# Kernel optimization log

Measured on AMD Instinct MI355X. Metric: run time of the kernel, lower is better.

## Reference

```python
import jax, jax.numpy as jnp
import numpy as np

EMBED_DIM = 1024
NUM_HEADS = 16
HEAD_DIM = EMBED_DIM // NUM_HEADS
B, S = 2, 2048


def setup_inputs() -> dict:
    key = jax.random.key(0)
    ks = jax.random.split(key, 9)
    d = EMBED_DIM
    std = 1.0 / np.sqrt(d)
    inp = {
        "x": jax.random.normal(ks[0], (B, S, d), dtype=jnp.float32),
        "wq": jax.random.normal(ks[1], (d, d), dtype=jnp.float32) * std,
        "bq": jnp.zeros((d,), dtype=jnp.float32),
        "wk": jax.random.normal(ks[2], (d, d), dtype=jnp.float32) * std,
        "bk": jnp.zeros((d,), dtype=jnp.float32),
        "wv": jax.random.normal(ks[3], (d, d), dtype=jnp.float32) * std,
        "bv": jnp.zeros((d,), dtype=jnp.float32),
        "wo": jax.random.normal(ks[4], (d, d), dtype=jnp.float32) * std,
        "bo": jnp.zeros((d,), dtype=jnp.float32),
    }
    return inp


def _split_heads(t):
    # [B,S,D] -> [B,H,S,hd]
    b, s, _ = t.shape
    return t.reshape(b, s, NUM_HEADS, HEAD_DIM).transpose(0, 2, 1, 3)


def reference(x, wq, bq, wk, bk, wv, bv, wo, bo):
    scaling = HEAD_DIM ** -0.5
    q = _split_heads(x @ wq + bq)
    k = _split_heads(x @ wk + bk)
    v = _split_heads(x @ wv + bv)
    # scaled dot-product attention, full [B,H,S,S] scores as in the torch code
    attn = jnp.einsum("bhqd,bhkd->bhqk", q, k) * scaling
    attn = jax.nn.softmax(attn, axis=-1)
    out = jnp.einsum("bhqk,bhkd->bhqd", attn, v)
    out = out.transpose(0, 2, 1, 3).reshape(x.shape[0], x.shape[1], EMBED_DIM)
    out = out @ wo + bo
    return out, attn
```

## Files before the change

### kernel.cpp

```cpp
#include <hip/hip_runtime.h>

#define B_   2
#define S_   2048
#define D_   1024
#define H_   16
#define HD_  64
#define MTOT 4096

typedef __bf16 bf16_t;
typedef bf16_t bf16x8 __attribute__((ext_vector_type(8)));
typedef bf16_t bf16x4 __attribute__((ext_vector_type(4)));
typedef float  f32x4  __attribute__((ext_vector_type(4)));

__device__ __forceinline__ void gl_lds16(const bf16_t* g, bf16_t* l) {
  __builtin_amdgcn_global_load_lds((const __attribute__((address_space(1))) void*)g,
                                   (__attribute__((address_space(3))) void*)l, 16, 0, 0);
}

__global__ void cvt_kernel(const float* __restrict__ in, bf16_t* __restrict__ o) {
  size_t i = ((size_t)blockIdx.x * 256 + threadIdx.x) * 4;
  float4 v = *(const float4*)(in + i);
  bf16x4 p;
  p[0] = (bf16_t)v.x; p[1] = (bf16_t)v.y; p[2] = (bf16_t)v.z; p[3] = (bf16_t)v.w;
  *(bf16x4*)(o + i) = p;
}

__global__ void transpose_kernel(const float* __restrict__ w0, const float* __restrict__ w1,
                                 const float* __restrict__ w2, const float* __restrict__ w3,
                                 bf16_t* __restrict__ t0, bf16_t* __restrict__ t1,
                                 bf16_t* __restrict__ t2, bf16_t* __restrict__ t3) {
  const float* w = blockIdx.z == 0 ? w0 : (blockIdx.z == 1 ? w1 : (blockIdx.z == 2 ? w2 : w3));
  bf16_t*      o = blockIdx.z == 0 ? t0 : (blockIdx.z == 1 ? t1 : (blockIdx.z == 2 ? t2 : t3));
  __shared__ float tile[32][33];
  int bx = blockIdx.x * 32, by = blockIdx.y * 32;
#pragma unroll
  for (int i = threadIdx.y; i < 32; i += 8)
    tile[i][threadIdx.x] = w[(size_t)(by + i) * D_ + bx + threadIdx.x];
  __syncthreads();
#pragma unroll
  for (int i = threadIdx.y; i < 32; i += 8)
    o[(size_t)(bx + i) * D_ + by + threadIdx.x] = (bf16_t)tile[threadIdx.x][i];
}

__device__ __forceinline__ void gemm_core(const bf16_t* __restrict__ A,
                                          const bf16_t* __restrict__ Bt,
                                          bf16_t* sA, bf16_t* sB,
                                          int bm, int bn, f32x4 acc[4][4]) {
  const int t = threadIdx.x;
  const int w = t >> 6, lane = t & 63;
  const int wr = w >> 1, wc = w & 1;
  const int r0 = w * 16 + (lane >> 2);
  const int kk = (lane & 3) * 8;
  const int fr = lane & 15, fg = lane >> 4;

  for (int k0 = 0; k0 < 1024; k0 += 32) {
    __syncthreads();
    gl_lds16(A  + (size_t)(bm + r0)      * 1024 + k0 + kk, sA + w * 512);
    gl_lds16(A  + (size_t)(bm + r0 + 64) * 1024 + k0 + kk, sA + 2048 + w * 512);
    gl_lds16(Bt + (size_t)(bn + r0)      * 1024 + k0 + kk, sB + w * 512);
    gl_lds16(Bt + (size_t)(bn + r0 + 64) * 1024 + k0 + kk, sB + 2048 + w * 512);
    __syncthreads();
    bf16x8 a[4], b[4];
#pragma unroll
    for (int m = 0; m < 4; ++m)
      a[m] = *(const bf16x8*)&sA[(wr * 64 + m * 16 + fr) * 32 + fg * 8];
#pragma unroll
    for (int n = 0; n < 4; ++n)
      b[n] = *(const bf16x8*)&sB[(wc * 64 + n * 16 + fr) * 32 + fg * 8];
#pragma unroll
    for (int m = 0; m < 4; ++m)
#pragma unroll
      for (int n = 0; n < 4; ++n)
        acc[m][n] = __builtin_amdgcn_mfma_f32_16x16x32_bf16(a[m], b[n], acc[m][n], 0, 0, 0);
  }
}

__global__ __launch_bounds__(256) void qkv_gemm(
    const bf16_t* __restrict__ xb,
    const bf16_t* __restrict__ wqT, const bf16_t* __restrict__ wkT, const bf16_t* __restrict__ wvT,
    const float* __restrict__ bq, const float* __restrict__ bk, const float* __restrict__ bv,
    bf16_t* __restrict__ Qb, bf16_t* __restrict__ Kb, bf16_t* __restrict__ Vt) {
  __shared__ bf16_t sA[128 * 32], sB[128 * 32];
  const int bid = blockIdx.x;
  const int nid = (bid & 7) * 96 + (bid >> 3);
  const int z = nid >> 8, rem = nid & 255;
  const int bm = (rem >> 3) * 128, bn = (rem & 7) * 128;
  const bf16_t* Bt   = z == 0 ? wqT : (z == 1 ? wkT : wvT);
  const float*  bias = z == 0 ? bq  : (z == 1 ? bk  : bv);

  f32x4 acc[4][4];
#pragma unroll
  for (int m = 0; m < 4; ++m)
#pragma unroll
    for (int n = 0; n < 4; ++n) acc[m][n] = (f32x4){0.f, 0.f, 0.f, 0.f};

  gemm_core(xb, Bt, sA, sB, bm, bn, acc);

  const int t = threadIdx.x, w = t >> 6, lane = t & 63;
  const int wr = w >> 1, wc = w & 1, fr = lane & 15, fg = lane >> 4;
  if (z <= 1) {
    bf16_t* O = (z == 0) ? Qb : Kb;
#pragma unroll
    for (int m = 0; m < 4; ++m)
#pragma unroll
      for (int n = 0; n < 4; ++n) {
        int col = bn + wc * 64 + n * 16 + fr;
        int h = col >> 6, d = col & 63;
        float bi = bias[col];
#pragma unroll
        for (int j = 0; j < 4; ++j) {
          int row = bm + wr * 64 + m * 16 + fg * 4 + j;
          int bb = row >> 11, s = row & 2047;
          O[(((size_t)(bb * H_ + h)) * S_ + s) * HD_ + d] = (bf16_t)(acc[m][n][j] + bi);
        }
      }
  } else {
#pragma unroll
    for (int m = 0; m < 4; ++m)
#pragma unroll
      for (int n = 0; n < 4; ++n) {
        int col = bn + wc * 64 + n * 16 + fr;
        int h = col >> 6, d = col & 63;
        float bi = bias[col];
        int row0 = bm + wr * 64 + m * 16 + fg * 4;
        int bb = row0 >> 11, s0 = row0 & 2047;
        bf16x4 pk;
#pragma unroll
        for (int j = 0; j < 4; ++j) pk[j] = (bf16_t)(acc[m][n][j] + bi);
        *(bf16x4*)&Vt[(((size_t)(bb * H_ + h)) * HD_ + d) * S_ + s0] = pk;
      }
  }
}

__global__ __launch_bounds__(256) void out_gemm(const bf16_t* __restrict__ Ob,
                                                const bf16_t* __restrict__ woT,
                                                const float* __restrict__ bo,
                                                float* __restrict__ out) {
  __shared__ bf16_t sA[128 * 32], sB[128 * 32];
  const int bid = blockIdx.x;
  const int nid = (bid & 7) * 32 + (bid >> 3);
  const int bm = (nid >> 3) * 128, bn = (nid & 7) * 128;
  f32x4 acc[4][4];
#pragma unroll
  for (int m = 0; m < 4; ++m)
#pragma unroll
    for (int n = 0; n < 4; ++n) acc[m][n] = (f32x4){0.f, 0.f, 0.f, 0.f};

  gemm_core(Ob, woT, sA, sB, bm, bn, acc);

  const int t = threadIdx.x, w = t >> 6, lane = t & 63;
  const int wr = w >> 1, wc = w & 1, fr = lane & 15, fg = lane >> 4;
#pragma unroll
  for (int m = 0; m < 4; ++m)
#pragma unroll
    for (int n = 0; n < 4; ++n) {
      int col = bn + wc * 64 + n * 16 + fr;
      float bi = bo[col];
#pragma unroll
      for (int j = 0; j < 4; ++j) {
        int row = bm + wr * 64 + m * 16 + fg * 4 + j;
        out[(size_t)row * D_ + col] = acc[m][n][j] + bi;
      }
    }
}

__global__ __launch_bounds__(256) void attn_kernel(const bf16_t* __restrict__ Qb,
                                                   const bf16_t* __restrict__ Kb,
                                                   const bf16_t* __restrict__ Vt,
                                                   float* __restrict__ attn,
                                                   bf16_t* __restrict__ Ob) {
  __shared__ bf16_t p_lds[4][16 * 72];
  const int t = threadIdx.x, w = t >> 6, lane = t & 63;
  const int fr = lane & 15, fg = lane >> 4;
  const int bid = blockIdx.x;
  const int nid = (bid & 7) * 128 + (bid >> 3);
  const int qblk = nid & 31, bh = nid >> 5;
  const int bb = bh >> 4, h = bh & 15;
  const int q0 = qblk * 64 + w * 16;

  const bf16_t* Qh = Qb + (size_t)bh * S_ * HD_;
  const bf16_t* Kh = Kb + (size_t)bh * S_ * HD_;
  const bf16_t* Vh = Vt + (size_t)bh * HD_ * S_;

  bf16x8 aq0 = *(const bf16x8*)&Qh[(size_t)(q0 + fr) * HD_ + fg * 8];
  bf16x8 aq1 = *(const bf16x8*)&Qh[(size_t)(q0 + fr) * HD_ + 32 + fg * 8];

  float lsum = 0.f;
  for (int kt = 0; kt < S_; kt += 64) {
#pragma unroll
    for (int c = 0; c < 4; ++c) {
      const bf16_t* kp = &Kh[(size_t)(kt + c * 16 + fr) * HD_ + fg * 8];
      bf16x8 kb0 = *(const bf16x8*)kp;
      bf16x8 kb1 = *(const bf16x8*)(kp + 32);
      f32x4 zz = {0.f, 0.f, 0.f, 0.f};
      __builtin_amdgcn_s_setprio(1);
      zz = __builtin_amdgcn_mfma_f32_16x16x32_bf16(kb0, aq0, zz, 0, 0, 0);
      zz = __builtin_amdgcn_mfma_f32_16x16x32_bf16(kb1, aq1, zz, 0, 0, 0);
      __builtin_amdgcn_s_setprio(0);
#pragma unroll
      for (int j = 0; j < 4; ++j) lsum += __expf(zz[j] * 0.125f);
    }
  }
  lsum += __shfl_xor(lsum, 16, 64);
  lsum += __shfl_xor(lsum, 32, 64);
  const float invq = 1.f / lsum;

  f32x4 oacc[4];
#pragma unroll
  for (int g = 0; g < 4; ++g) oacc[g] = (f32x4){0.f, 0.f, 0.f, 0.f};

  float* attn_base = attn + ((size_t)bh * S_ + q0) * S_;
  for (int kt = 0; kt < S_; kt += 64) {
#pragma unroll
    for (int c = 0; c < 4; ++c) {
      const bf16_t* kp = &Kh[(size_t)(kt + c * 16 + fr) * HD_ + fg * 8];
      bf16x8 kb0 = *(const bf16x8*)kp;
      bf16x8 kb1 = *(const bf16x8*)(kp + 32);
      f32x4 zz = {0.f, 0.f, 0.f, 0.f};
      __builtin_amdgcn_s_setprio(1);
      zz = __builtin_amdgcn_mfma_f32_16x16x32_bf16(kb0, aq0, zz, 0, 0, 0);
      zz = __builtin_amdgcn_mfma_f32_16x16x32_bf16(kb1, aq1, zz, 0, 0, 0);
      __builtin_amdgcn_s_setprio(0);
      f32x4 pv;
      bf16x4 pk;
#pragma unroll
      for (int j = 0; j < 4; ++j) {
        float p = __expf(zz[j] * 0.125f) * invq;
        pv[j] = p; pk[j] = (bf16_t)p;
      }
      *(f32x4*)&attn_base[(size_t)fr * S_ + kt + c * 16 + fg * 4] = pv;
      *(bf16x4*)&p_lds[w][fr * 72 + c * 16 + fg * 4] = pk;
    }
    bf16x8 ap0 = *(const bf16x8*)&p_lds[w][fr * 72 + fg * 8];
    bf16x8 ap1 = *(const bf16x8*)&p_lds[w][fr * 72 + 32 + fg * 8];
#pragma unroll
    for (int g = 0; g < 4; ++g) {
      const bf16_t* vp = &Vh[(size_t)(g * 16 + fr) * S_ + kt + fg * 8];
      bf16x8 b0 = *(const bf16x8*)vp;
      bf16x8 b1 = *(const bf16x8*)(vp + 32);
      __builtin_amdgcn_s_setprio(1);
      oacc[g] = __builtin_amdgcn_mfma_f32_16x16x32_bf16(ap0, b0, oacc[g], 0, 0, 0);
      oacc[g] = __builtin_amdgcn_mfma_f32_16x16x32_bf16(ap1, b1, oacc[g], 0, 0, 0);
      __builtin_amdgcn_s_setprio(0);
    }
  }

#pragma unroll
  for (int g = 0; g < 4; ++g)
#pragma unroll
    for (int j = 0; j < 4; ++j) {
      int s = q0 + fg * 4 + j;
      Ob[((size_t)bb * S_ + s) * D_ + h * HD_ + g * 16 + fr] = (bf16_t)oacc[g][j];
    }
}

extern "C" void kernel_launch(void* const* d_in, const int* in_sizes, int n_in,
                              void* d_out, int out_size, void* d_ws, size_t ws_size,
                              hipStream_t stream) {
  const float* x  = (const float*)d_in[0];
  const float* wq = (const float*)d_in[1];
  const float* bq = (const float*)d_in[2];
  const float* wk = (const float*)d_in[3];
  const float* bk = (const float*)d_in[4];
  const float* wv = (const float*)d_in[5];
  const float* bv = (const float*)d_in[6];
  const float* wo = (const float*)d_in[7];
  const float* bo = (const float*)d_in[8];

  float* out  = (float*)d_out;
  float* attn = out + (size_t)B_ * S_ * D_;

  char* ws = (char*)d_ws;
  bf16_t* xb  = (bf16_t*)(ws);
  bf16_t* wqT = (bf16_t*)(ws + (size_t)( 8 << 20));
  bf16_t* wkT = (bf16_t*)(ws + (size_t)(10 << 20));
  bf16_t* wvT = (bf16_t*)(ws + (size_t)(12 << 20));
  bf16_t* woT = (bf16_t*)(ws + (size_t)(14 << 20));
  bf16_t* Qb  = (bf16_t*)(ws + (size_t)(16 << 20));
  bf16_t* Kb  = (bf16_t*)(ws + (size_t)(24 << 20));
  bf16_t* Vt  = (bf16_t*)(ws + (size_t)(32 << 20));
  bf16_t* Ob  = (bf16_t*)(ws + (size_t)(40 << 20));

  cvt_kernel<<<4096, 256, 0, stream>>>(x, xb);
  transpose_kernel<<<dim3(32, 32, 4), dim3(32, 8), 0, stream>>>(wq, wk, wv, wo, wqT, wkT, wvT, woT);
  qkv_gemm<<<768, 256, 0, stream>>>(xb, wqT, wkT, wvT, bq, bk, bv, Qb, Kb, Vt);
  attn_kernel<<<1024, 256, 0, stream>>>(Qb, Kb, Vt, attn, Ob);
  out_gemm<<<256, 256, 0, stream>>>(Ob, woT, bo, out);
}
```

Measured before the change: 986.6 us.

## Stage 256-key probability tiles in LDS and store attn rows coalesced

The PV loop now covers 256 keys per outer step. Each wave writes bf16 probabilities for 16 query rows into a wider LDS tile, then runs eight MFMAs per output group against V. The fp32 attention matrix is no longer written as scattered 16-byte pieces from the MFMA fragment layout. Instead, each row is read back from LDS and stored with full-wave contiguous writes, which targets the dominant global write traffic. The trade-off is that the stored attention probabilities are now bf16-rounded values widened back to fp32, which lowers output precision and uses more LDS per block.

```diff
diff --git a/kernel.cpp b/kernel.cpp
--- a/kernel.cpp
+++ b/kernel.cpp
@@ -169,7 +169,7 @@
                                                    const bf16_t* __restrict__ Vt,
                                                    float* __restrict__ attn,
                                                    bf16_t* __restrict__ Ob) {
-  __shared__ bf16_t p_lds[4][16 * 72];
+  __shared__ bf16_t p_lds[4][16 * 264];
   const int t = threadIdx.x, w = t >> 6, lane = t & 63;
   const int fr = lane & 15, fg = lane >> 4;
   const int bid = blockIdx.x;
@@ -209,39 +209,47 @@
 #pragma unroll
   for (int g = 0; g < 4; ++g) oacc[g] = (f32x4){0.f, 0.f, 0.f, 0.f};
 
+  bf16_t* pw = &p_lds[w][0];
   float* attn_base = attn + ((size_t)bh * S_ + q0) * S_;
-  for (int kt = 0; kt < S_; kt += 64) {
-#pragma unroll
-    for (int c = 0; c < 4; ++c) {
-      const bf16_t* kp = &Kh[(size_t)(kt + c * 16 + fr) * HD_ + fg * 8];
-      bf16x8 kb0 = *(const bf16x8*)kp;
-      bf16x8 kb1 = *(const bf16x8*)(kp + 32);
-      f32x4 zz = {0.f, 0.f, 0.f, 0.f};
+  for (int KT = 0; KT < S_; KT += 256) {
+#pragma unroll
+    for (int c64 = 0; c64 < 4; ++c64) {
+      const int kt = KT + c64 * 64;
+#pragma unroll
+      for (int c = 0; c < 4; ++c) {
+        const bf16_t* kp = &Kh[(size_t)(kt + c * 16 + fr) * HD_ + fg * 8];
+        bf16x8 kb0 = *(const bf16x8*)kp;
+        bf16x8 kb1 = *(const bf16x8*)(kp + 32);
+        f32x4 zz = {0.f, 0.f, 0.f, 0.f};
+        __builtin_amdgcn_s_setprio(1);
+        zz = __builtin_amdgcn_mfma_f32_16x16x32_bf16(kb0, aq0, zz, 0, 0, 0);
+        zz = __builtin_amdgcn_mfma_f32_16x16x32_bf16(kb1, aq1, zz, 0, 0, 0);
+        __builtin_amdgcn_s_setprio(0);
+        bf16x4 pk;
+#pragma unroll
+        for (int j = 0; j < 4; ++j) pk[j] = (bf16_t)(__expf(zz[j] * 0.125f) * invq);
+        *(bf16x4*)&pw[fr * 264 + c64 * 64 + c * 16 + fg * 4] = pk;
+      }
+    }
+#pragma unroll
+    for (int g = 0; g < 4; ++g) {
+      const bf16_t* vrow = &Vh[(size_t)(g * 16 + fr) * S_ + KT + fg * 8];
       __builtin_amdgcn_s_setprio(1);
-      zz = __builtin_amdgcn_mfma_f32_16x16x32_bf16(kb0, aq0, zz, 0, 0, 0);
-      zz = __builtin_amdgcn_mfma_f32_16x16x32_bf16(kb1, aq1, zz, 0, 0, 0);
+#pragma unroll
+      for (int ks = 0; ks < 8; ++ks) {
+        bf16x8 ap = *(const bf16x8*)&pw[fr * 264 + ks * 32 + fg * 8];
+        bf16x8 vb = *(const bf16x8*)(vrow + ks * 32);
+        oacc[g] = __builtin_amdgcn_mfma_f32_16x16x32_bf16(ap, vb, oacc[g], 0, 0, 0);
+      }
       __builtin_amdgcn_s_setprio(0);
+    }
+#pragma unroll
+    for (int i = 0; i < 16; ++i) {
+      bf16x4 pk = *(const bf16x4*)&pw[i * 264 + lane * 4];
       f32x4 pv;
-      bf16x4 pk;
-#pragma unroll
-      for (int j = 0; j < 4; ++j) {
-        float p = __expf(zz[j] * 0.125f) * invq;
-        pv[j] = p; pk[j] = (bf16_t)p;
-      }
-      *(f32x4*)&attn_base[(size_t)fr * S_ + kt + c * 16 + fg * 4] = pv;
-      *(bf16x4*)&p_lds[w][fr * 72 + c * 16 + fg * 4] = pk;
-    }
-    bf16x8 ap0 = *(const bf16x8*)&p_lds[w][fr * 72 + fg * 8];
-    bf16x8 ap1 = *(const bf16x8*)&p_lds[w][fr * 72 + 32 + fg * 8];
-#pragma unroll
-    for (int g = 0; g < 4; ++g) {
-      const bf16_t* vp = &Vh[(size_t)(g * 16 + fr) * S_ + kt + fg * 8];
-      bf16x8 b0 = *(const bf16x8*)vp;
-      bf16x8 b1 = *(const bf16x8*)(vp + 32);
-      __builtin_amdgcn_s_setprio(1);
-      oacc[g] = __builtin_amdgcn_mfma_f32_16x16x32_bf16(ap0, b0, oacc[g], 0, 0, 0);
-      oacc[g] = __builtin_amdgcn_mfma_f32_16x16x32_bf16(ap1, b1, oacc[g], 0, 0, 0);
-      __builtin_amdgcn_s_setprio(0);
+#pragma unroll
+      for (int j = 0; j < 4; ++j) pv[j] = (float)pk[j];
+      *(f32x4*)&attn_base[(size_t)i * S_ + KT + lane * 4] = pv;
     }
   }
 
```

Result: faster. 916.3 us (-7.1%).
